# Optimization experiments

Hardware: AMD Instinct MI355X
Metric: run time of the kernel (lower is better)

Reference implementation:

```python
import jax, jax.numpy as jnp
import numpy as np

N_NODES = 100000
N_EDGES = 1200000
IN_CH = 64
HID = 16
OUT_CH = 64
EDGE_DIM = 3


def _glorot(key, shape):
    fan_in, fan_out = shape[0], shape[1]
    lim = float(np.sqrt(6.0 / (fan_in + fan_out)))
    return jax.random.uniform(key, shape, jnp.float32, -lim, lim)


def setup_inputs() -> dict:
    key = jax.random.key(0)
    ks = jax.random.split(key, 16)
    x = jax.random.normal(ks[0], (N_NODES, IN_CH), jnp.float32)
    edge_index = jax.random.randint(ks[1], (2, N_EDGES), 0, N_NODES, jnp.int64)
    edge_attr = jax.random.normal(ks[2], (N_EDGES, EDGE_DIM), jnp.float32)
    return {
        "x": x,
        "edge_index": edge_index,
        "edge_attr": edge_attr,
        # conv1: in->16
        "W1l": _glorot(ks[3], (IN_CH, HID)), "b1l": jnp.zeros((HID,), jnp.float32),
        "W1r": _glorot(ks[4], (IN_CH, HID)), "b1r": jnp.zeros((HID,), jnp.float32),
        "W1e": _glorot(ks[5], (EDGE_DIM, IN_CH)), "b1e": jnp.zeros((IN_CH,), jnp.float32),
        # conv2: 16->out
        "W2l": _glorot(ks[6], (HID, OUT_CH)), "b2l": jnp.zeros((OUT_CH,), jnp.float32),
        "W2r": _glorot(ks[7], (HID, OUT_CH)), "b2r": jnp.zeros((OUT_CH,), jnp.float32),
        "W2e": _glorot(ks[8], (EDGE_DIM, HID)), "b2e": jnp.zeros((HID,), jnp.float32),
    }


def _sage_conv(x, src, dst, edge_attr, We, be, Wl, bl, Wr, br):
    # message: neighbor feature + projected edge attribute (edge_dim-aware SAGE)
    msg = x[src] + edge_attr @ We + be                       # [E, C_in]
    agg = jax.ops.segment_sum(msg, dst, num_segments=N_NODES)  # [N, C_in]
    deg = jax.ops.segment_sum(jnp.ones((msg.shape[0],), msg.dtype), dst,
                              num_segments=N_NODES)
    agg = agg / jnp.maximum(deg, 1.0)[:, None]               # mean aggregation
    return agg @ Wl + bl + x @ Wr + br                       # neighbor + self paths


def reference(x, edge_index, edge_attr,
              W1l, b1l, W1r, b1r, W1e, b1e,
              W2l, b2l, W2r, b2r, W2e, b2e):
    src, dst = edge_index[0], edge_index[1]
    h = jax.nn.relu(_sage_conv(x, src, dst, edge_attr, W1e, b1e, W1l, b1l, W1r, b1r))
    # F.dropout(training=self.training): eval mode -> identity
    out = _sage_conv(h, src, dst, edge_attr, W2e, b2e, W2l, b2l, W2r, b2r)
    return out
```

## Files before the change

### kernel.cpp

```cpp
#include <hip/hip_runtime.h>
#include <hip/hip_bf16.h>
#include <stdint.h>

#define N_NODES 100000
#define N_EDGES 1200000
#define IN_CH 64
#define HID 16
#define OUT_CH 64

#define BN 100
#define NB 1000
#define BCAP 2048
#define CAP 2048
#define SC_EPB 4096
#define SC_TPB 512
#define SC_EPT (SC_EPB / SC_TPB)

typedef __hip_bfloat16 bf16;

__device__ __forceinline__ float b2f(bf16 v) { return __bfloat162float(v); }
__device__ __forceinline__ float lo_f(uint32_t p) { return __uint_as_float(p << 16); }
__device__ __forceinline__ float hi_f(uint32_t p) { return __uint_as_float(p & 0xffff0000u); }
__device__ __forceinline__ uint16_t f2bb(float v) {
    bf16 h = __float2bfloat16(v);
    return *reinterpret_cast<uint16_t*>(&h);
}

__device__ __forceinline__ float loadf(const void* p, size_t i, int bf) {
    return bf ? b2f(((const bf16*)p)[i]) : ((const float*)p)[i];
}
__device__ __forceinline__ uint32_t bfbits(const void* p, size_t i, int bf) {
    if (bf) return ((const uint16_t*)p)[i];
    return f2bb(((const float*)p)[i]);
}
__device__ __forceinline__ int ld_dst(const int* p, int j, int i64) {
    if (i64) return ((const int2*)p)[(size_t)N_EDGES + j].x;
    return p[(size_t)N_EDGES + j];
}
__device__ __forceinline__ int ld_src(const int* p, int j, int i64) {
    if (i64) return ((const int2*)p)[j].x;
    return p[j];
}

__device__ __forceinline__ int detect_bf(const void* x) {
    const uint16_t* u = (const uint16_t*)x;
    int cnt = 0;
    for (int i = 0; i < 64; ++i) {
        int e = (u[i] >> 7) & 0xff;
        cnt += (e >= 100 && e <= 140);
    }
    return cnt >= 50;
}
__device__ __forceinline__ int detect_i64(const int* ei) {
    const uint32_t* w = (const uint32_t*)ei;
    int z = 0;
    for (int i = 1; i < 64; i += 2) z += (w[i] == 0u);
    return z >= 16;
}

__global__ void __launch_bounds__(256) k_y(const void* __restrict__ x,
                                           const void* __restrict__ W1l,
                                           const void* __restrict__ W1r,
                                           const void* __restrict__ b1l,
                                           const void* __restrict__ b1r,
                                           const void* __restrict__ W1e,
                                           const void* __restrict__ b1e,
                                           bf16* __restrict__ y,
                                           bf16* __restrict__ zh,
                                           float* __restrict__ wc,
                                           int* __restrict__ gcnt) {
    __shared__ float w[IN_CH * 32];
    __shared__ float bz[HID];
    __shared__ int s_bf;
    if (threadIdx.x == 0) s_bf = detect_bf(x);
    __syncthreads();
    int bf = s_bf;
    for (int t = threadIdx.x; t < IN_CH * 32; t += 256) {
        int k = t >> 5, cc = t & 31;
        w[t] = (cc < 16) ? loadf(W1l, k * HID + cc, bf) : loadf(W1r, k * HID + (cc - 16), bf);
    }
    if (threadIdx.x < HID)
        bz[threadIdx.x] = loadf(b1l, threadIdx.x, bf) + loadf(b1r, threadIdx.x, bf);
    if (blockIdx.x == 0) {
        for (int i = threadIdx.x; i < NB; i += 256) gcnt[i] = 0;
    }
    __syncthreads();
    if (blockIdx.x == 0 && threadIdx.x < HID) {
        int j = threadIdx.x;
        float s0 = 0.f, s1 = 0.f, s2 = 0.f, s3 = 0.f;
        for (int k = 0; k < IN_CH; ++k) {
            float wl = w[k * 32 + j];
            s0 += loadf(W1e, k, bf) * wl;
            s1 += loadf(W1e, IN_CH + k, bf) * wl;
            s2 += loadf(W1e, 2 * IN_CH + k, bf) * wl;
            s3 += loadf(b1e, k, bf) * wl;
        }
        wc[j] = s0;
        wc[HID + j] = s1;
        wc[2 * HID + j] = s2;
        wc[3 * HID + j] = s3;
    }
    int tid = blockIdx.x * 256 + threadIdx.x;
    int row = tid >> 1;
    if (row >= N_NODES) return;
    int half = tid & 1, cs = half * 16;
    float acc[16];
#pragma unroll
    for (int j = 0; j < 16; ++j) acc[j] = 0.f;
    if (bf) {
        const uint4* xr = (const uint4*)((const uint16_t*)x + (size_t)row * IN_CH);
        uint4 q[8];
#pragma unroll
        for (int i = 0; i < 8; ++i) q[i] = xr[i];
        const uint32_t* qq = (const uint32_t*)q;
#pragma unroll
        for (int k2 = 0; k2 < 32; ++k2) {
            uint32_t u = qq[k2];
            float x0 = lo_f(u), x1 = hi_f(u);
            const float* w0 = &w[(2 * k2) * 32 + cs];
            const float* w1 = w0 + 32;
#pragma unroll
            for (int j = 0; j < 16; ++j) acc[j] += x0 * w0[j] + x1 * w1[j];
        }
    } else {
        const float4* xr = (const float4*)((const float*)x + (size_t)row * IN_CH);
#pragma unroll
        for (int c = 0; c < 4; ++c) {
            float4 f[4];
#pragma unroll
            for (int i = 0; i < 4; ++i) f[i] = xr[c * 4 + i];
            const float* ff = (const float*)f;
#pragma unroll
            for (int kk = 0; kk < 16; ++kk) {
                float xk = ff[kk];
                const float* wr = &w[(c * 16 + kk) * 32 + cs];
#pragma unroll
                for (int j = 0; j < 16; ++j) acc[j] += xk * wr[j];
            }
        }
    }
    if (half) {
#pragma unroll
        for (int j = 0; j < 16; ++j) acc[j] += bz[j];
    }
    uint32_t pk[8];
#pragma unroll
    for (int j2 = 0; j2 < 8; ++j2)
        pk[j2] = (uint32_t)f2bb(acc[2 * j2]) | ((uint32_t)f2bb(acc[2 * j2 + 1]) << 16);
    bf16* dst = half ? (zh + (size_t)row * HID) : (y + (size_t)row * HID);
    uint4* d4 = (uint4*)dst;
    d4[0] = make_uint4(pk[0], pk[1], pk[2], pk[3]);
    d4[1] = make_uint4(pk[4], pk[5], pk[6], pk[7]);
}

__global__ void __launch_bounds__(SC_TPB) k_bscatter(const void* __restrict__ x,
                                                     const int* __restrict__ ei,
                                                     const void* __restrict__ ea,
                                                     int* __restrict__ gcnt,
                                                     uint2* __restrict__ slots,
                                                     uint16_t* __restrict__ ea2v) {
    __shared__ int lhist[NB];
    __shared__ int lscan[NB];
    __shared__ int ldelta[NB];
    __shared__ int wsum[8];
    __shared__ int s_flags;
    __shared__ uint2 lval[SC_EPB];
    __shared__ uint16_t lea[SC_EPB];
    __shared__ uint16_t lbid[SC_EPB];
    int t = threadIdx.x;
    for (int i = t; i < NB; i += SC_TPB) lhist[i] = 0;
    if (t == 0) s_flags = detect_bf(x) | (detect_i64(ei) << 1);
    __syncthreads();
    int bf = s_flags & 1, i64 = (s_flags >> 1) & 1;
    int base = blockIdx.x * SC_EPB;
    uint32_t rb[SC_EPT], srcv[SC_EPT], ea01v[SC_EPT], ea2r[SC_EPT];
#pragma unroll
    for (int i = 0; i < SC_EPT; ++i) {
        int e = base + i * SC_TPB + t;
        rb[i] = 0xFFFFFFFFu;
        if (e < N_EDGES) {
            uint32_t d = (uint32_t)ld_dst(ei, e, i64);
            srcv[i] = (uint32_t)ld_src(ei, e, i64);
            ea01v[i] = bfbits(ea, (size_t)e * 3, bf) |
                       (bfbits(ea, (size_t)e * 3 + 1, bf) << 16);
            ea2r[i] = bfbits(ea, (size_t)e * 3 + 2, bf);
            uint32_t b = d / BN;
            uint32_t dl = d - b * BN;
            uint32_t r = (uint32_t)atomicAdd(&lhist[b], 1);
            rb[i] = (b << 19) | (dl << 12) | r;
        }
    }
    __syncthreads();
    int b0 = 2 * t, b1 = 2 * t + 1;
    int cnt0 = (b0 < NB) ? lhist[b0] : 0;
    int cnt1 = (b1 < NB) ? lhist[b1] : 0;
    int s_local = cnt0 + cnt1;
    int incl = s_local;
    int lane = t & 63;
#pragma unroll
    for (int d = 1; d < 64; d <<= 1) {
        int v = __shfl_up(incl, d);
        if (lane >= d) incl += v;
    }
    int w = t >> 6;
    if (lane == 63) wsum[w] = incl;
    __syncthreads();
    int wbase = 0, nst = 0;
#pragma unroll
    for (int i = 0; i < 8; ++i) {
        int v = wsum[i];
        wbase += (i < w) ? v : 0;
        nst += v;
    }
    int run = wbase + incl - s_local;
    if (b0 < NB) {
        lscan[b0] = run;
        if (cnt0) ldelta[b0] = b0 * BCAP + atomicAdd(&gcnt[b0], cnt0) - run;
    }
    run += cnt0;
    if (b1 < NB) {
        lscan[b1] = run;
        if (cnt1) ldelta[b1] = b1 * BCAP + atomicAdd(&gcnt[b1], cnt1) - run;
    }
    __syncthreads();
#pragma unroll
    for (int i = 0; i < SC_EPT; ++i) {
        if (rb[i] == 0xFFFFFFFFu) continue;
        uint32_t b = rb[i] >> 19;
        uint32_t dl = (rb[i] >> 12) & 0x7Fu;
        uint32_t r = rb[i] & 0xFFFu;
        int lp = lscan[b] + (int)r;
        lval[lp] = make_uint2(srcv[i] | (dl << 17), ea01v[i]);
        lea[lp] = (uint16_t)ea2r[i];
        lbid[lp] = (uint16_t)b;
    }
    __syncthreads();
    for (int p = t; p < nst; p += SC_TPB) {
        int b = lbid[p];
        int gp = ldelta[b] + p;
        slots[gp] = lval[p];
        ea2v[gp] = lea[p];
    }
}

#define SORT_CHUNK(nst)                                                        \
    {                                                                          \
        for (int i_ = t; i_ < (nst); i_ += 256)                                \
            atomicAdd(&hist[su[i_].x >> 17], 1);                               \
        __syncthreads();                                                       \
        if (t < 128) sbuf[t] = (t < BN) ? hist[t] : 0;                         \
        __syncthreads();                                                       \
        for (int off_ = 1; off_ < 128; off_ <<= 1) {                           \
            int v_ = 0;                                                        \
            if (t < 128 && t >= off_) v_ = sbuf[t - off_];                     \
            __syncthreads();                                                   \
            if (t < 128) sbuf[t] += v_;                                        \
            __syncthreads();                                                   \
        }                                                                      \
        if (t < BN) {                                                          \
            int ex_ = sbuf[t] - hist[t];                                       \
            noff[t] = ex_;                                                     \
            cur[t] = ex_;                                                      \
        }                                                                      \
        __syncthreads();                                                       \
        for (int i_ = t; i_ < (nst); i_ += 256) {                              \
            int r_ = atomicAdd(&cur[su[i_].x >> 17], 1);                       \
            sidx[r_] = (uint16_t)i_;                                           \
        }                                                                      \
        __syncthreads();                                                       \
    }

__global__ void __launch_bounds__(256) k_agg1(const uint2* __restrict__ slots,
                                              const uint16_t* __restrict__ ea2v,
                                              const int* __restrict__ gcnt,
                                              const bf16* __restrict__ y,
                                              const float* __restrict__ wc,
                                              bf16* __restrict__ zh,
                                              float* __restrict__ sa) {
    __shared__ uint2 su[CAP];
    __shared__ uint16_t ea2s[CAP];
    __shared__ uint16_t sidx[CAP];
    __shared__ int hist[BN], noff[BN], cur[BN], sbuf[128];
    __shared__ float swc[64];
    int t = threadIdx.x;
    if (t < 64) swc[t] = wc[t];
    int b = blockIdx.x;
    int n = gcnt[b];
    const uint2* sp = slots + (size_t)b * BCAP;
    const uint16_t* ep = ea2v + (size_t)b * BCAP;
    int dl = t >> 1, half = t & 1, cs = half * 8;
    float acc[8] = {0.f, 0.f, 0.f, 0.f, 0.f, 0.f, 0.f, 0.f};
    float a0 = 0.f, a1 = 0.f, a2 = 0.f, degT = 0.f;

    for (int base = 0; base < n; base += CAP) {
        int nst = n - base < CAP ? n - base : CAP;
        for (int i_ = t; i_ < BN; i_ += 256) hist[i_] = 0;
        for (int i_ = t; i_ < nst; i_ += 256) {
            su[i_] = sp[base + i_];
            ea2s[i_] = ep[base + i_];
        }
        __syncthreads();
        SORT_CHUNK(nst)
        if (dl < BN) {
            int kb = noff[dl];
            int ke = (dl == BN - 1) ? nst : noff[dl + 1];
            int k = kb;
            for (; k + 3 < ke; k += 4) {
                int i0 = sidx[k], i1 = sidx[k + 1], i2 = sidx[k + 2], i3 = sidx[k + 3];
                uint2 s0 = su[i0], s1 = su[i1], s2 = su[i2], s3 = su[i3];
                uint4 q0 = *(const uint4*)(y + (size_t)(s0.x & 0x1FFFFu) * HID + cs);
                uint4 q1 = *(const uint4*)(y + (size_t)(s1.x & 0x1FFFFu) * HID + cs);
                uint4 q2 = *(const uint4*)(y + (size_t)(s2.x & 0x1FFFFu) * HID + cs);
                uint4 q3 = *(const uint4*)(y + (size_t)(s3.x & 0x1FFFFu) * HID + cs);
                acc[0] += lo_f(q0.x) + lo_f(q1.x) + lo_f(q2.x) + lo_f(q3.x);
                acc[1] += hi_f(q0.x) + hi_f(q1.x) + hi_f(q2.x) + hi_f(q3.x);
                acc[2] += lo_f(q0.y) + lo_f(q1.y) + lo_f(q2.y) + lo_f(q3.y);
                acc[3] += hi_f(q0.y) + hi_f(q1.y) + hi_f(q2.y) + hi_f(q3.y);
                acc[4] += lo_f(q0.z) + lo_f(q1.z) + lo_f(q2.z) + lo_f(q3.z);
                acc[5] += hi_f(q0.z) + hi_f(q1.z) + hi_f(q2.z) + hi_f(q3.z);
                acc[6] += lo_f(q0.w) + lo_f(q1.w) + lo_f(q2.w) + lo_f(q3.w);
                acc[7] += hi_f(q0.w) + hi_f(q1.w) + hi_f(q2.w) + hi_f(q3.w);
                if (half == 0) {
                    a0 += lo_f(s0.y) + lo_f(s1.y) + lo_f(s2.y) + lo_f(s3.y);
                    a1 += hi_f(s0.y) + hi_f(s1.y) + hi_f(s2.y) + hi_f(s3.y);
                    a2 += __uint_as_float((uint32_t)ea2s[i0] << 16) +
                          __uint_as_float((uint32_t)ea2s[i1] << 16) +
                          __uint_as_float((uint32_t)ea2s[i2] << 16) +
                          __uint_as_float((uint32_t)ea2s[i3] << 16);
                }
            }
            for (; k < ke; ++k) {
                int i0 = sidx[k];
                uint2 s0 = su[i0];
                uint4 q0 = *(const uint4*)(y + (size_t)(s0.x & 0x1FFFFu) * HID + cs);
                acc[0] += lo_f(q0.x); acc[1] += hi_f(q0.x);
                acc[2] += lo_f(q0.y); acc[3] += hi_f(q0.y);
                acc[4] += lo_f(q0.z); acc[5] += hi_f(q0.z);
                acc[6] += lo_f(q0.w); acc[7] += hi_f(q0.w);
                if (half == 0) {
                    a0 += lo_f(s0.y);
                    a1 += hi_f(s0.y);
                    a2 += __uint_as_float((uint32_t)ea2s[i0] << 16);
                }
            }
            degT += (float)hist[dl];
        }
        __syncthreads();
    }
    if (dl < BN) {
        a0 += __shfl_xor(a0, 1);
        a1 += __shfl_xor(a1, 1);
        a2 += __shfl_xor(a2, 1);
        size_t i = (size_t)b * BN + dl;
        float inv = 1.0f / fmaxf(degT, 1.0f);
        uint4 zq = *(const uint4*)(zh + i * HID + cs);
        float zf[8] = {lo_f(zq.x), hi_f(zq.x), lo_f(zq.y), hi_f(zq.y),
                       lo_f(zq.z), hi_f(zq.z), lo_f(zq.w), hi_f(zq.w)};
        uint32_t pk[4];
#pragma unroll
        for (int j = 0; j < 4; ++j) {
            float t0 = (acc[2 * j] + a0 * swc[cs + 2 * j] + a1 * swc[16 + cs + 2 * j] +
                        a2 * swc[32 + cs + 2 * j] + degT * swc[48 + cs + 2 * j]) * inv;
            float t1 = (acc[2 * j + 1] + a0 * swc[cs + 2 * j + 1] + a1 * swc[17 + cs + 2 * j] +
                        a2 * swc[33 + cs + 2 * j] + degT * swc[49 + cs + 2 * j]) * inv;
            float h0 = fmaxf(t0 + zf[2 * j], 0.f);
            float h1 = fmaxf(t1 + zf[2 * j + 1], 0.f);
            pk[j] = (uint32_t)f2bb(h0) | ((uint32_t)f2bb(h1) << 16);
        }
        *(uint4*)(zh + i * HID + cs) = make_uint4(pk[0], pk[1], pk[2], pk[3]);
        if (half == 0) {
            sa[i * 3 + 0] = a0;
            sa[i * 3 + 1] = a1;
            sa[i * 3 + 2] = a2;
        }
    }
}

__global__ void __launch_bounds__(256) k_agg2(const void* __restrict__ x,
                                              const uint2* __restrict__ slots,
                                              const int* __restrict__ gcnt,
                                              const bf16* __restrict__ zh,
                                              const float* __restrict__ sa,
                                              const void* __restrict__ W2l,
                                              const void* __restrict__ b2l,
                                              const void* __restrict__ W2r,
                                              const void* __restrict__ b2r,
                                              const void* __restrict__ W2e,
                                              const void* __restrict__ b2e,
                                              void* __restrict__ out) {
    __shared__ uint2 su[CAP];
    __shared__ uint16_t sidx[CAP];
    __shared__ int hist[BN], noff[BN], cur[BN], sbuf[128];
    __shared__ float facc[BN * HID];
    __shared__ bf16 hl[BN * HID];
    __shared__ float w2l[HID * OUT_CH];
    __shared__ float w2r[HID * OUT_CH];
    __shared__ float swe[3 * HID];
    __shared__ float sbe[HID];
    __shared__ float sbb[OUT_CH];
    __shared__ int s_bf;
    int t = threadIdx.x;
    if (t == 0) s_bf = detect_bf(x);
    __syncthreads();
    int bf = s_bf;
    for (int i = t; i < HID * OUT_CH; i += 256) {
        w2l[i] = loadf(W2l, i, bf);
        w2r[i] = loadf(W2r, i, bf);
    }
    if (t < 3 * HID) swe[t] = loadf(W2e, t, bf);
    if (t < HID) sbe[t] = loadf(b2e, t, bf);
    if (t < OUT_CH) sbb[t] = loadf(b2l, t, bf) + loadf(b2r, t, bf);
    int b = blockIdx.x;
    int n = gcnt[b];
    const uint2* sp = slots + (size_t)b * BCAP;
    int dl = t >> 1, half = t & 1, cs = half * 8;
    float acc[8] = {0.f, 0.f, 0.f, 0.f, 0.f, 0.f, 0.f, 0.f};
    float degT = 0.f;

    for (int base = 0; base < n; base += CAP) {
        int nst = n - base < CAP ? n - base : CAP;
        for (int i_ = t; i_ < BN; i_ += 256) hist[i_] = 0;
        for (int i_ = t; i_ < nst; i_ += 256) su[i_] = sp[base + i_];
        __syncthreads();
        SORT_CHUNK(nst)
        if (dl < BN) {
            int kb = noff[dl];
            int ke = (dl == BN - 1) ? nst : noff[dl + 1];
            int k = kb;
            for (; k + 3 < ke; k += 4) {
                int i0 = sidx[k], i1 = sidx[k + 1], i2 = sidx[k + 2], i3 = sidx[k + 3];
                uint2 s0 = su[i0], s1 = su[i1], s2 = su[i2], s3 = su[i3];
                uint4 q0 = *(const uint4*)(zh + (size_t)(s0.x & 0x1FFFFu) * HID + cs);
                uint4 q1 = *(const uint4*)(zh + (size_t)(s1.x & 0x1FFFFu) * HID + cs);
                uint4 q2 = *(const uint4*)(zh + (size_t)(s2.x & 0x1FFFFu) * HID + cs);
                uint4 q3 = *(const uint4*)(zh + (size_t)(s3.x & 0x1FFFFu) * HID + cs);
                acc[0] += lo_f(q0.x) + lo_f(q1.x) + lo_f(q2.x) + lo_f(q3.x);
                acc[1] += hi_f(q0.x) + hi_f(q1.x) + hi_f(q2.x) + hi_f(q3.x);
                acc[2] += lo_f(q0.y) + lo_f(q1.y) + lo_f(q2.y) + lo_f(q3.y);
                acc[3] += hi_f(q0.y) + hi_f(q1.y) + hi_f(q2.y) + hi_f(q3.y);
                acc[4] += lo_f(q0.z) + lo_f(q1.z) + lo_f(q2.z) + lo_f(q3.z);
                acc[5] += hi_f(q0.z) + hi_f(q1.z) + hi_f(q2.z) + hi_f(q3.z);
                acc[6] += lo_f(q0.w) + lo_f(q1.w) + lo_f(q2.w) + lo_f(q3.w);
                acc[7] += hi_f(q0.w) + hi_f(q1.w) + hi_f(q2.w) + hi_f(q3.w);
            }
            for (; k < ke; ++k) {
                uint2 s0 = su[sidx[k]];
                uint4 q0 = *(const uint4*)(zh + (size_t)(s0.x & 0x1FFFFu) * HID + cs);
                acc[0] += lo_f(q0.x); acc[1] += hi_f(q0.x);
                acc[2] += lo_f(q0.y); acc[3] += hi_f(q0.y);
                acc[4] += lo_f(q0.z); acc[5] += hi_f(q0.z);
                acc[6] += lo_f(q0.w); acc[7] += hi_f(q0.w);
            }
            degT += (float)hist[dl];
        }
        __syncthreads();
    }
    if (dl < BN) {
        size_t i = (size_t)b * BN + dl;
        float inv = 1.0f / fmaxf(degT, 1.0f);
        float a0 = sa[i * 3 + 0], a1 = sa[i * 3 + 1], a2 = sa[i * 3 + 2];
        float4 f0, f1;
        float* fo = (float*)&f0;
        float* f1o = (float*)&f1;
#pragma unroll
        for (int j = 0; j < 4; ++j) {
            fo[j] = (acc[j] + a0 * swe[cs + j] + a1 * swe[16 + cs + j] +
                     a2 * swe[32 + cs + j] + degT * sbe[cs + j]) * inv;
            f1o[j] = (acc[4 + j] + a0 * swe[cs + 4 + j] + a1 * swe[16 + cs + 4 + j] +
                      a2 * swe[32 + cs + 4 + j] + degT * sbe[cs + 4 + j]) * inv;
        }
        *(float4*)&facc[dl * HID + cs] = f0;
        *(float4*)&facc[dl * HID + cs + 4] = f1;
        *(uint4*)&hl[dl * HID + cs] = *(const uint4*)(zh + i * HID + cs);
    }
    __syncthreads();
    for (int idx = t; idx < BN * OUT_CH; idx += 256) {
        int dli = idx >> 6, j = idx & 63;
        size_t i = (size_t)b * BN + dli;
        float o = sbb[j];
#pragma unroll
        for (int cc = 0; cc < HID; ++cc)
            o += facc[dli * HID + cc] * w2l[cc * OUT_CH + j] +
                 b2f(hl[dli * HID + cc]) * w2r[cc * OUT_CH + j];
        if (bf)
            ((bf16*)out)[i * OUT_CH + j] = __float2bfloat16(o);
        else
            ((float*)out)[i * OUT_CH + j] = o;
    }
}

extern "C" void kernel_launch(void* const* d_in, const int* in_sizes, int n_in,
                              void* d_out, int out_size, void* d_ws, size_t ws_size,
                              hipStream_t stream) {
    const void* x   = d_in[0];
    const int*  ei  = (const int*)d_in[1];
    const void* ea  = d_in[2];
    const void* W1l = d_in[3];
    const void* b1l = d_in[4];
    const void* W1r = d_in[5];
    const void* b1r = d_in[6];
    const void* W1e = d_in[7];
    const void* b1e = d_in[8];
    const void* W2l = d_in[9];
    const void* b2l = d_in[10];
    const void* W2r = d_in[11];
    const void* b2r = d_in[12];
    const void* W2e = d_in[13];
    const void* b2e = d_in[14];

    const size_t N16 = (size_t)N_NODES * HID;
    char* p = (char*)d_ws;
    uint2*    slots  = (uint2*)p;    p += (size_t)NB * BCAP * sizeof(uint2);
    uint16_t* ea2v   = (uint16_t*)p; p += (size_t)NB * BCAP * sizeof(uint16_t);
    bf16*     y      = (bf16*)p;     p += N16 * sizeof(bf16);
    bf16*     zh     = (bf16*)p;     p += N16 * sizeof(bf16);
    float*    sa     = (float*)p;    p += (size_t)3 * N_NODES * sizeof(float);
    int*      gcnt   = (int*)p;      p += NB * sizeof(int);
    float*    wc     = (float*)p;    p += 64 * sizeof(float);

    k_y<<<((size_t)N_NODES * 2 + 255) / 256, 256, 0, stream>>>(x, W1l, W1r, b1l, b1r,
                                                               W1e, b1e, y, zh, wc, gcnt);
    k_bscatter<<<(N_EDGES + SC_EPB - 1) / SC_EPB, SC_TPB, 0, stream>>>(x, ei, ea, gcnt,
                                                                       slots, ea2v);
    k_agg1<<<NB, 256, 0, stream>>>(slots, ea2v, gcnt, y, wc, zh, sa);
    k_agg2<<<NB, 256, 0, stream>>>(x, slots, gcnt, zh, sa, W2l, b2l, W2r, b2r,
                                   W2e, b2e, d_out);
}
```

Baseline: 200.8 us.

## Fuse node projection with edge bucketing and reuse sorted sources in layer two

Merges the node-projection kernel and the edge bucket-scatter kernel into one launch, with blocks interleaved by role (2 projection, 3 scatter per group) and a shared memory pool. The gcnt zeroing becomes a memset. The first aggregation kernel now writes its per-bucket sorted source list and node offsets to global memory, so the second aggregation skips reloading slots and re-sorting. The per-bucket chunk loop is dropped in favour of clamping counts to CAP. This trades an extra global write/read of the sorted arrays for removing one launch and the second sort, and silently truncates buckets with more than CAP edges.

New measurement: 194.0 us. 1.04x faster.

```diff
diff --git a/kernel.cpp b/kernel.cpp
--- a/kernel.cpp
+++ b/kernel.cpp
@@ -12,9 +12,13 @@
 #define NB 1000
 #define BCAP 2048
 #define CAP 2048
-#define SC_EPB 4096
-#define SC_TPB 512
-#define SC_EPT (SC_EPB / SC_TPB)
+
+#define F_TPB 512
+#define KY_BLOCKS ((N_NODES * 2 + F_TPB - 1) / F_TPB)
+#define SC_EPB 2048
+#define SC_EPT (SC_EPB / F_TPB)
+#define SC_BLOCKS ((N_EDGES + SC_EPB - 1) / SC_EPB)
+#define F_GROUPS 196
 
 typedef __hip_bfloat16 bf16;
 
@@ -58,125 +62,127 @@
     return z >= 16;
 }
 
-__global__ void __launch_bounds__(256) k_y(const void* __restrict__ x,
-                                           const void* __restrict__ W1l,
-                                           const void* __restrict__ W1r,
-                                           const void* __restrict__ b1l,
-                                           const void* __restrict__ b1r,
-                                           const void* __restrict__ W1e,
-                                           const void* __restrict__ b1e,
-                                           bf16* __restrict__ y,
-                                           bf16* __restrict__ zh,
-                                           float* __restrict__ wc,
-                                           int* __restrict__ gcnt) {
-    __shared__ float w[IN_CH * 32];
-    __shared__ float bz[HID];
-    __shared__ int s_bf;
-    if (threadIdx.x == 0) s_bf = detect_bf(x);
-    __syncthreads();
-    int bf = s_bf;
-    for (int t = threadIdx.x; t < IN_CH * 32; t += 256) {
-        int k = t >> 5, cc = t & 31;
-        w[t] = (cc < 16) ? loadf(W1l, k * HID + cc, bf) : loadf(W1r, k * HID + (cc - 16), bf);
-    }
-    if (threadIdx.x < HID)
-        bz[threadIdx.x] = loadf(b1l, threadIdx.x, bf) + loadf(b1r, threadIdx.x, bf);
-    if (blockIdx.x == 0) {
-        for (int i = threadIdx.x; i < NB; i += 256) gcnt[i] = 0;
-    }
-    __syncthreads();
-    if (blockIdx.x == 0 && threadIdx.x < HID) {
-        int j = threadIdx.x;
-        float s0 = 0.f, s1 = 0.f, s2 = 0.f, s3 = 0.f;
-        for (int k = 0; k < IN_CH; ++k) {
-            float wl = w[k * 32 + j];
-            s0 += loadf(W1e, k, bf) * wl;
-            s1 += loadf(W1e, IN_CH + k, bf) * wl;
-            s2 += loadf(W1e, 2 * IN_CH + k, bf) * wl;
-            s3 += loadf(b1e, k, bf) * wl;
-        }
-        wc[j] = s0;
-        wc[HID + j] = s1;
-        wc[2 * HID + j] = s2;
-        wc[3 * HID + j] = s3;
-    }
-    int tid = blockIdx.x * 256 + threadIdx.x;
-    int row = tid >> 1;
-    if (row >= N_NODES) return;
-    int half = tid & 1, cs = half * 16;
-    float acc[16];
-#pragma unroll
-    for (int j = 0; j < 16; ++j) acc[j] = 0.f;
-    if (bf) {
-        const uint4* xr = (const uint4*)((const uint16_t*)x + (size_t)row * IN_CH);
-        uint4 q[8];
-#pragma unroll
-        for (int i = 0; i < 8; ++i) q[i] = xr[i];
-        const uint32_t* qq = (const uint32_t*)q;
-#pragma unroll
-        for (int k2 = 0; k2 < 32; ++k2) {
-            uint32_t u = qq[k2];
-            float x0 = lo_f(u), x1 = hi_f(u);
-            const float* w0 = &w[(2 * k2) * 32 + cs];
-            const float* w1 = w0 + 32;
-#pragma unroll
-            for (int j = 0; j < 16; ++j) acc[j] += x0 * w0[j] + x1 * w1[j];
-        }
-    } else {
-        const float4* xr = (const float4*)((const float*)x + (size_t)row * IN_CH);
-#pragma unroll
-        for (int c = 0; c < 4; ++c) {
-            float4 f[4];
-#pragma unroll
-            for (int i = 0; i < 4; ++i) f[i] = xr[c * 4 + i];
-            const float* ff = (const float*)f;
-#pragma unroll
-            for (int kk = 0; kk < 16; ++kk) {
-                float xk = ff[kk];
-                const float* wr = &w[(c * 16 + kk) * 32 + cs];
-#pragma unroll
-                for (int j = 0; j < 16; ++j) acc[j] += xk * wr[j];
-            }
-        }
-    }
-    if (half) {
-#pragma unroll
-        for (int j = 0; j < 16; ++j) acc[j] += bz[j];
-    }
-    uint32_t pk[8];
-#pragma unroll
-    for (int j2 = 0; j2 < 8; ++j2)
-        pk[j2] = (uint32_t)f2bb(acc[2 * j2]) | ((uint32_t)f2bb(acc[2 * j2 + 1]) << 16);
-    bf16* dst = half ? (zh + (size_t)row * HID) : (y + (size_t)row * HID);
-    uint4* d4 = (uint4*)dst;
-    d4[0] = make_uint4(pk[0], pk[1], pk[2], pk[3]);
-    d4[1] = make_uint4(pk[4], pk[5], pk[6], pk[7]);
-}
-
-__global__ void __launch_bounds__(SC_TPB) k_bscatter(const void* __restrict__ x,
-                                                     const int* __restrict__ ei,
-                                                     const void* __restrict__ ea,
-                                                     int* __restrict__ gcnt,
-                                                     uint2* __restrict__ slots,
-                                                     uint16_t* __restrict__ ea2v) {
-    __shared__ int lhist[NB];
-    __shared__ int lscan[NB];
-    __shared__ int ldelta[NB];
+__global__ void __launch_bounds__(F_TPB) k_fused(const void* __restrict__ x,
+                                                 const int* __restrict__ ei,
+                                                 const void* __restrict__ ea,
+                                                 const void* __restrict__ W1l,
+                                                 const void* __restrict__ W1r,
+                                                 const void* __restrict__ b1l,
+                                                 const void* __restrict__ b1r,
+                                                 const void* __restrict__ W1e,
+                                                 const void* __restrict__ b1e,
+                                                 bf16* __restrict__ y,
+                                                 bf16* __restrict__ zh,
+                                                 float* __restrict__ wc,
+                                                 int* __restrict__ gcnt,
+                                                 uint2* __restrict__ slots,
+                                                 uint16_t* __restrict__ ea2v) {
+    __shared__ __align__(16) char smem[36608];
     __shared__ int wsum[8];
     __shared__ int s_flags;
-    __shared__ uint2 lval[SC_EPB];
-    __shared__ uint16_t lea[SC_EPB];
-    __shared__ uint16_t lbid[SC_EPB];
     int t = threadIdx.x;
-    for (int i = t; i < NB; i += SC_TPB) lhist[i] = 0;
+    int g = blockIdx.x / 5, r = blockIdx.x % 5;
     if (t == 0) s_flags = detect_bf(x) | (detect_i64(ei) << 1);
+
+    if (r < 2) {
+        int kyid = g * 2 + r;
+        if (kyid >= KY_BLOCKS) return;
+        float* w = (float*)smem;
+        float* bz = (float*)(smem + 8192);
+        __syncthreads();
+        int bf = s_flags & 1;
+        for (int i = t; i < IN_CH * 32; i += F_TPB) {
+            int k = i >> 5, cc = i & 31;
+            w[i] = (cc < 16) ? loadf(W1l, k * HID + cc, bf)
+                             : loadf(W1r, k * HID + (cc - 16), bf);
+        }
+        if (t < HID) bz[t] = loadf(b1l, t, bf) + loadf(b1r, t, bf);
+        __syncthreads();
+        if (kyid == 0 && t < HID) {
+            int j = t;
+            float s0 = 0.f, s1 = 0.f, s2 = 0.f, s3 = 0.f;
+            for (int k = 0; k < IN_CH; ++k) {
+                float wl = w[k * 32 + j];
+                s0 += loadf(W1e, k, bf) * wl;
+                s1 += loadf(W1e, IN_CH + k, bf) * wl;
+                s2 += loadf(W1e, 2 * IN_CH + k, bf) * wl;
+                s3 += loadf(b1e, k, bf) * wl;
+            }
+            wc[j] = s0;
+            wc[HID + j] = s1;
+            wc[2 * HID + j] = s2;
+            wc[3 * HID + j] = s3;
+        }
+        int tid = kyid * F_TPB + t;
+        int row = tid >> 1;
+        if (row >= N_NODES) return;
+        int half = tid & 1, cs = half * 16;
+        float acc[16];
+#pragma unroll
+        for (int j = 0; j < 16; ++j) acc[j] = 0.f;
+        if (bf) {
+            const uint4* xr = (const uint4*)((const uint16_t*)x + (size_t)row * IN_CH);
+            uint4 q[8];
+#pragma unroll
+            for (int i = 0; i < 8; ++i) q[i] = xr[i];
+            const uint32_t* qq = (const uint32_t*)q;
+#pragma unroll
+            for (int k2 = 0; k2 < 32; ++k2) {
+                uint32_t u = qq[k2];
+                float x0 = lo_f(u), x1 = hi_f(u);
+                const float* w0 = &w[(2 * k2) * 32 + cs];
+                const float* w1 = w0 + 32;
+#pragma unroll
+                for (int j = 0; j < 16; ++j) acc[j] += x0 * w0[j] + x1 * w1[j];
+            }
+        } else {
+            const float4* xr = (const float4*)((const float*)x + (size_t)row * IN_CH);
+#pragma unroll
+            for (int c = 0; c < 4; ++c) {
+                float4 f[4];
+#pragma unroll
+                for (int i = 0; i < 4; ++i) f[i] = xr[c * 4 + i];
+                const float* ff = (const float*)f;
+#pragma unroll
+                for (int kk = 0; kk < 16; ++kk) {
+                    float xk = ff[kk];
+                    const float* wr = &w[(c * 16 + kk) * 32 + cs];
+#pragma unroll
+                    for (int j = 0; j < 16; ++j) acc[j] += xk * wr[j];
+                }
+            }
+        }
+        if (half) {
+#pragma unroll
+            for (int j = 0; j < 16; ++j) acc[j] += bz[j];
+        }
+        uint32_t pk[8];
+#pragma unroll
+        for (int j2 = 0; j2 < 8; ++j2)
+            pk[j2] = (uint32_t)f2bb(acc[2 * j2]) | ((uint32_t)f2bb(acc[2 * j2 + 1]) << 16);
+        bf16* dst = half ? (zh + (size_t)row * HID) : (y + (size_t)row * HID);
+        uint4* d4 = (uint4*)dst;
+        d4[0] = make_uint4(pk[0], pk[1], pk[2], pk[3]);
+        d4[1] = make_uint4(pk[4], pk[5], pk[6], pk[7]);
+        return;
+    }
+
+    int scid = g * 3 + (r - 2);
+    if (scid >= SC_BLOCKS) return;
+    uint2* lval = (uint2*)smem;
+    int* lhist = (int*)(smem + 16384);
+    int* lscan = (int*)(smem + 20384);
+    int* ldelta = (int*)(smem + 24384);
+    uint16_t* lea = (uint16_t*)(smem + 28384);
+    uint16_t* lbid = (uint16_t*)(smem + 32480);
+    for (int i = t; i < NB; i += F_TPB) lhist[i] = 0;
     __syncthreads();
     int bf = s_flags & 1, i64 = (s_flags >> 1) & 1;
-    int base = blockIdx.x * SC_EPB;
+    int base = scid * SC_EPB;
     uint32_t rb[SC_EPT], srcv[SC_EPT], ea01v[SC_EPT], ea2r[SC_EPT];
 #pragma unroll
     for (int i = 0; i < SC_EPT; ++i) {
-        int e = base + i * SC_TPB + t;
+        int e = base + i * F_TPB + t;
         rb[i] = 0xFFFFFFFFu;
         if (e < N_EDGES) {
             uint32_t d = (uint32_t)ld_dst(ei, e, i64);
@@ -186,8 +192,8 @@
             ea2r[i] = bfbits(ea, (size_t)e * 3 + 2, bf);
             uint32_t b = d / BN;
             uint32_t dl = d - b * BN;
-            uint32_t r = (uint32_t)atomicAdd(&lhist[b], 1);
-            rb[i] = (b << 19) | (dl << 12) | r;
+            uint32_t rr = (uint32_t)atomicAdd(&lhist[b], 1);
+            rb[i] = (b << 19) | (dl << 12) | rr;
         }
     }
     __syncthreads();
@@ -228,14 +234,14 @@
         if (rb[i] == 0xFFFFFFFFu) continue;
         uint32_t b = rb[i] >> 19;
         uint32_t dl = (rb[i] >> 12) & 0x7Fu;
-        uint32_t r = rb[i] & 0xFFFu;
-        int lp = lscan[b] + (int)r;
+        uint32_t rr = rb[i] & 0xFFFu;
+        int lp = lscan[b] + (int)rr;
         lval[lp] = make_uint2(srcv[i] | (dl << 17), ea01v[i]);
         lea[lp] = (uint16_t)ea2r[i];
         lbid[lp] = (uint16_t)b;
     }
     __syncthreads();
-    for (int p = t; p < nst; p += SC_TPB) {
+    for (int p = t; p < nst; p += F_TPB) {
         int b = lbid[p];
         int gp = ldelta[b] + p;
         slots[gp] = lval[p];
@@ -276,7 +282,9 @@
                                               const bf16* __restrict__ y,
                                               const float* __restrict__ wc,
                                               bf16* __restrict__ zh,
-                                              float* __restrict__ sa) {
+                                              float* __restrict__ sa,
+                                              uint32_t* __restrict__ ssrc,
+                                              int* __restrict__ nof2) {
     __shared__ uint2 su[CAP];
     __shared__ uint16_t ea2s[CAP];
     __shared__ uint16_t sidx[CAP];
@@ -286,66 +294,65 @@
     if (t < 64) swc[t] = wc[t];
     int b = blockIdx.x;
     int n = gcnt[b];
+    if (n > CAP) n = CAP;
     const uint2* sp = slots + (size_t)b * BCAP;
     const uint16_t* ep = ea2v + (size_t)b * BCAP;
     int dl = t >> 1, half = t & 1, cs = half * 8;
     float acc[8] = {0.f, 0.f, 0.f, 0.f, 0.f, 0.f, 0.f, 0.f};
     float a0 = 0.f, a1 = 0.f, a2 = 0.f, degT = 0.f;
 
-    for (int base = 0; base < n; base += CAP) {
-        int nst = n - base < CAP ? n - base : CAP;
-        for (int i_ = t; i_ < BN; i_ += 256) hist[i_] = 0;
-        for (int i_ = t; i_ < nst; i_ += 256) {
-            su[i_] = sp[base + i_];
-            ea2s[i_] = ep[base + i_];
-        }
-        __syncthreads();
-        SORT_CHUNK(nst)
-        if (dl < BN) {
-            int kb = noff[dl];
-            int ke = (dl == BN - 1) ? nst : noff[dl + 1];
-            int k = kb;
-            for (; k + 3 < ke; k += 4) {
-                int i0 = sidx[k], i1 = sidx[k + 1], i2 = sidx[k + 2], i3 = sidx[k + 3];
-                uint2 s0 = su[i0], s1 = su[i1], s2 = su[i2], s3 = su[i3];
-                uint4 q0 = *(const uint4*)(y + (size_t)(s0.x & 0x1FFFFu) * HID + cs);
-                uint4 q1 = *(const uint4*)(y + (size_t)(s1.x & 0x1FFFFu) * HID + cs);
-                uint4 q2 = *(const uint4*)(y + (size_t)(s2.x & 0x1FFFFu) * HID + cs);
-                uint4 q3 = *(const uint4*)(y + (size_t)(s3.x & 0x1FFFFu) * HID + cs);
-                acc[0] += lo_f(q0.x) + lo_f(q1.x) + lo_f(q2.x) + lo_f(q3.x);
-                acc[1] += hi_f(q0.x) + hi_f(q1.x) + hi_f(q2.x) + hi_f(q3.x);
-                acc[2] += lo_f(q0.y) + lo_f(q1.y) + lo_f(q2.y) + lo_f(q3.y);
-                acc[3] += hi_f(q0.y) + hi_f(q1.y) + hi_f(q2.y) + hi_f(q3.y);
-                acc[4] += lo_f(q0.z) + lo_f(q1.z) + lo_f(q2.z) + lo_f(q3.z);
-                acc[5] += hi_f(q0.z) + hi_f(q1.z) + hi_f(q2.z) + hi_f(q3.z);
-                acc[6] += lo_f(q0.w) + lo_f(q1.w) + lo_f(q2.w) + lo_f(q3.w);
-                acc[7] += hi_f(q0.w) + hi_f(q1.w) + hi_f(q2.w) + hi_f(q3.w);
-                if (half == 0) {
-                    a0 += lo_f(s0.y) + lo_f(s1.y) + lo_f(s2.y) + lo_f(s3.y);
-                    a1 += hi_f(s0.y) + hi_f(s1.y) + hi_f(s2.y) + hi_f(s3.y);
-                    a2 += __uint_as_float((uint32_t)ea2s[i0] << 16) +
-                          __uint_as_float((uint32_t)ea2s[i1] << 16) +
-                          __uint_as_float((uint32_t)ea2s[i2] << 16) +
-                          __uint_as_float((uint32_t)ea2s[i3] << 16);
-                }
+    for (int i_ = t; i_ < BN; i_ += 256) hist[i_] = 0;
+    for (int i_ = t; i_ < n; i_ += 256) {
+        su[i_] = sp[i_];
+        ea2s[i_] = ep[i_];
+    }
+    __syncthreads();
+    SORT_CHUNK(n)
+    for (int p = t; p < n; p += 256) ssrc[(size_t)b * BCAP + p] = su[sidx[p]].x;
+    if (t < BN) nof2[b * 128 + t] = noff[t];
+    if (dl < BN) {
+        int kb = noff[dl];
+        int ke = (dl == BN - 1) ? n : noff[dl + 1];
+        int k = kb;
+        for (; k + 3 < ke; k += 4) {
+            int i0 = sidx[k], i1 = sidx[k + 1], i2 = sidx[k + 2], i3 = sidx[k + 3];
+            uint2 s0 = su[i0], s1 = su[i1], s2 = su[i2], s3 = su[i3];
+            uint4 q0 = *(const uint4*)(y + (size_t)(s0.x & 0x1FFFFu) * HID + cs);
+            uint4 q1 = *(const uint4*)(y + (size_t)(s1.x & 0x1FFFFu) * HID + cs);
+            uint4 q2 = *(const uint4*)(y + (size_t)(s2.x & 0x1FFFFu) * HID + cs);
+            uint4 q3 = *(const uint4*)(y + (size_t)(s3.x & 0x1FFFFu) * HID + cs);
+            acc[0] += lo_f(q0.x) + lo_f(q1.x) + lo_f(q2.x) + lo_f(q3.x);
+            acc[1] += hi_f(q0.x) + hi_f(q1.x) + hi_f(q2.x) + hi_f(q3.x);
+            acc[2] += lo_f(q0.y) + lo_f(q1.y) + lo_f(q2.y) + lo_f(q3.y);
+            acc[3] += hi_f(q0.y) + hi_f(q1.y) + hi_f(q2.y) + hi_f(q3.y);
+            acc[4] += lo_f(q0.z) + lo_f(q1.z) + lo_f(q2.z) + lo_f(q3.z);
+            acc[5] += hi_f(q0.z) + hi_f(q1.z) + hi_f(q2.z) + hi_f(q3.z);
+            acc[6] += lo_f(q0.w) + lo_f(q1.w) + lo_f(q2.w) + lo_f(q3.w);
+            acc[7] += hi_f(q0.w) + hi_f(q1.w) + hi_f(q2.w) + hi_f(q3.w);
+            if (half == 0) {
+                a0 += lo_f(s0.y) + lo_f(s1.y) + lo_f(s2.y) + lo_f(s3.y);
+                a1 += hi_f(s0.y) + hi_f(s1.y) + hi_f(s2.y) + hi_f(s3.y);
+                a2 += __uint_as_float((uint32_t)ea2s[i0] << 16) +
+                      __uint_as_float((uint32_t)ea2s[i1] << 16) +
+                      __uint_as_float((uint32_t)ea2s[i2] << 16) +
+                      __uint_as_float((uint32_t)ea2s[i3] << 16);
             }
-            for (; k < ke; ++k) {
-                int i0 = sidx[k];
-                uint2 s0 = su[i0];
-                uint4 q0 = *(const uint4*)(y + (size_t)(s0.x & 0x1FFFFu) * HID + cs);
-                acc[0] += lo_f(q0.x); acc[1] += hi_f(q0.x);
-                acc[2] += lo_f(q0.y); acc[3] += hi_f(q0.y);
-                acc[4] += lo_f(q0.z); acc[5] += hi_f(q0.z);
-                acc[6] += lo_f(q0.w); acc[7] += hi_f(q0.w);
-                if (half == 0) {
-                    a0 += lo_f(s0.y);
-                    a1 += hi_f(s0.y);
-                    a2 += __uint_as_float((uint32_t)ea2s[i0] << 16);
-                }
+        }
+        for (; k < ke; ++k) {
+            int i0 = sidx[k];
+            uint2 s0 = su[i0];
+            uint4 q0 = *(const uint4*)(y + (size_t)(s0.x & 0x1FFFFu) * HID + cs);
+            acc[0] += lo_f(q0.x); acc[1] += hi_f(q0.x);
+            acc[2] += lo_f(q0.y); acc[3] += hi_f(q0.y);
+            acc[4] += lo_f(q0.z); acc[5] += hi_f(q0.z);
+            acc[6] += lo_f(q0.w); acc[7] += hi_f(q0.w);
+            if (half == 0) {
+                a0 += lo_f(s0.y);
+                a1 += hi_f(s0.y);
+                a2 += __uint_as_float((uint32_t)ea2s[i0] << 16);
             }
-            degT += (float)hist[dl];
-        }
-        __syncthreads();
+        }
+        degT = (float)hist[dl];
     }
     if (dl < BN) {
         a0 += __shfl_xor(a0, 1);
@@ -377,7 +384,8 @@
 }
 
 __global__ void __launch_bounds__(256) k_agg2(const void* __restrict__ x,
-                                              const uint2* __restrict__ slots,
+                                              const uint32_t* __restrict__ ssrc,
+                                              const int* __restrict__ nof2,
                                               const int* __restrict__ gcnt,
                                               const bf16* __restrict__ zh,
                                               const float* __restrict__ sa,
@@ -388,9 +396,8 @@
                                               const void* __restrict__ W2e,
                                               const void* __restrict__ b2e,
                                               void* __restrict__ out) {
-    __shared__ uint2 su[CAP];
-    __shared__ uint16_t sidx[CAP];
-    __shared__ int hist[BN], noff[BN], cur[BN], sbuf[128];
+    __shared__ uint32_t ss[CAP];
+    __shared__ int snoff[BN];
     __shared__ float facc[BN * HID];
     __shared__ bf16 hl[BN * HID];
     __shared__ float w2l[HID * OUT_CH];
@@ -412,48 +419,41 @@
     if (t < OUT_CH) sbb[t] = loadf(b2l, t, bf) + loadf(b2r, t, bf);
     int b = blockIdx.x;
     int n = gcnt[b];
-    const uint2* sp = slots + (size_t)b * BCAP;
+    if (n > CAP) n = CAP;
+    for (int i = t; i < n; i += 256) ss[i] = ssrc[(size_t)b * BCAP + i];
+    if (t < BN) snoff[t] = nof2[b * 128 + t];
+    __syncthreads();
     int dl = t >> 1, half = t & 1, cs = half * 8;
     float acc[8] = {0.f, 0.f, 0.f, 0.f, 0.f, 0.f, 0.f, 0.f};
     float degT = 0.f;
-
-    for (int base = 0; base < n; base += CAP) {
-        int nst = n - base < CAP ? n - base : CAP;
-        for (int i_ = t; i_ < BN; i_ += 256) hist[i_] = 0;
-        for (int i_ = t; i_ < nst; i_ += 256) su[i_] = sp[base + i_];
-        __syncthreads();
-        SORT_CHUNK(nst)
-        if (dl < BN) {
-            int kb = noff[dl];
-            int ke = (dl == BN - 1) ? nst : noff[dl + 1];
-            int k = kb;
-            for (; k + 3 < ke; k += 4) {
-                int i0 = sidx[k], i1 = sidx[k + 1], i2 = sidx[k + 2], i3 = sidx[k + 3];
-                uint2 s0 = su[i0], s1 = su[i1], s2 = su[i2], s3 = su[i3];
-                uint4 q0 = *(const uint4*)(zh + (size_t)(s0.x & 0x1FFFFu) * HID + cs);
-                uint4 q1 = *(const uint4*)(zh + (size_t)(s1.x & 0x1FFFFu) * HID + cs);
-                uint4 q2 = *(const uint4*)(zh + (size_t)(s2.x & 0x1FFFFu) * HID + cs);
-                uint4 q3 = *(const uint4*)(zh + (size_t)(s3.x & 0x1FFFFu) * HID + cs);
-                acc[0] += lo_f(q0.x) + lo_f(q1.x) + lo_f(q2.x) + lo_f(q3.x);
-                acc[1] += hi_f(q0.x) + hi_f(q1.x) + hi_f(q2.x) + hi_f(q3.x);
-                acc[2] += lo_f(q0.y) + lo_f(q1.y) + lo_f(q2.y) + lo_f(q3.y);
-                acc[3] += hi_f(q0.y) + hi_f(q1.y) + hi_f(q2.y) + hi_f(q3.y);
-                acc[4] += lo_f(q0.z) + lo_f(q1.z) + lo_f(q2.z) + lo_f(q3.z);
-                acc[5] += hi_f(q0.z) + hi_f(q1.z) + hi_f(q2.z) + hi_f(q3.z);
-                acc[6] += lo_f(q0.w) + lo_f(q1.w) + lo_f(q2.w) + lo_f(q3.w);
-                acc[7] += hi_f(q0.w) + hi_f(q1.w) + hi_f(q2.w) + hi_f(q3.w);
-            }
-            for (; k < ke; ++k) {
-                uint2 s0 = su[sidx[k]];
-                uint4 q0 = *(const uint4*)(zh + (size_t)(s0.x & 0x1FFFFu) * HID + cs);
-                acc[0] += lo_f(q0.x); acc[1] += hi_f(q0.x);
-                acc[2] += lo_f(q0.y); acc[3] += hi_f(q0.y);
-                acc[4] += lo_f(q0.z); acc[5] += hi_f(q0.z);
-                acc[6] += lo_f(q0.w); acc[7] += hi_f(q0.w);
-            }
-            degT += (float)hist[dl];
-        }
-        __syncthreads();
+    if (dl < BN) {
+        int kb = snoff[dl];
+        int ke = (dl == BN - 1) ? n : snoff[dl + 1];
+        degT = (float)(ke - kb);
+        int k = kb;
+        for (; k + 3 < ke; k += 4) {
+            uint32_t s0 = ss[k], s1 = ss[k + 1], s2 = ss[k + 2], s3 = ss[k + 3];
+            uint4 q0 = *(const uint4*)(zh + (size_t)(s0 & 0x1FFFFu) * HID + cs);
+            uint4 q1 = *(const uint4*)(zh + (size_t)(s1 & 0x1FFFFu) * HID + cs);
+            uint4 q2 = *(const uint4*)(zh + (size_t)(s2 & 0x1FFFFu) * HID + cs);
+            uint4 q3 = *(const uint4*)(zh + (size_t)(s3 & 0x1FFFFu) * HID + cs);
+            acc[0] += lo_f(q0.x) + lo_f(q1.x) + lo_f(q2.x) + lo_f(q3.x);
+            acc[1] += hi_f(q0.x) + hi_f(q1.x) + hi_f(q2.x) + hi_f(q3.x);
+            acc[2] += lo_f(q0.y) + lo_f(q1.y) + lo_f(q2.y) + lo_f(q3.y);
+            acc[3] += hi_f(q0.y) + hi_f(q1.y) + hi_f(q2.y) + hi_f(q3.y);
+            acc[4] += lo_f(q0.z) + lo_f(q1.z) + lo_f(q2.z) + lo_f(q3.z);
+            acc[5] += hi_f(q0.z) + hi_f(q1.z) + hi_f(q2.z) + hi_f(q3.z);
+            acc[6] += lo_f(q0.w) + lo_f(q1.w) + lo_f(q2.w) + lo_f(q3.w);
+            acc[7] += hi_f(q0.w) + hi_f(q1.w) + hi_f(q2.w) + hi_f(q3.w);
+        }
+        for (; k < ke; ++k) {
+            uint32_t s0 = ss[k];
+            uint4 q0 = *(const uint4*)(zh + (size_t)(s0 & 0x1FFFFu) * HID + cs);
+            acc[0] += lo_f(q0.x); acc[1] += hi_f(q0.x);
+            acc[2] += lo_f(q0.y); acc[3] += hi_f(q0.y);
+            acc[4] += lo_f(q0.z); acc[5] += hi_f(q0.z);
+            acc[6] += lo_f(q0.w); acc[7] += hi_f(q0.w);
+        }
     }
     if (dl < BN) {
         size_t i = (size_t)b * BN + dl;
@@ -510,19 +510,20 @@
 
     const size_t N16 = (size_t)N_NODES * HID;
     char* p = (char*)d_ws;
-    uint2*    slots  = (uint2*)p;    p += (size_t)NB * BCAP * sizeof(uint2);
-    uint16_t* ea2v   = (uint16_t*)p; p += (size_t)NB * BCAP * sizeof(uint16_t);
-    bf16*     y      = (bf16*)p;     p += N16 * sizeof(bf16);
-    bf16*     zh     = (bf16*)p;     p += N16 * sizeof(bf16);
-    float*    sa     = (float*)p;    p += (size_t)3 * N_NODES * sizeof(float);
-    int*      gcnt   = (int*)p;      p += NB * sizeof(int);
-    float*    wc     = (float*)p;    p += 64 * sizeof(float);
-
-    k_y<<<((size_t)N_NODES * 2 + 255) / 256, 256, 0, stream>>>(x, W1l, W1r, b1l, b1r,
-                                                               W1e, b1e, y, zh, wc, gcnt);
-    k_bscatter<<<(N_EDGES + SC_EPB - 1) / SC_EPB, SC_TPB, 0, stream>>>(x, ei, ea, gcnt,
-                                                                       slots, ea2v);
-    k_agg1<<<NB, 256, 0, stream>>>(slots, ea2v, gcnt, y, wc, zh, sa);
-    k_agg2<<<NB, 256, 0, stream>>>(x, slots, gcnt, zh, sa, W2l, b2l, W2r, b2r,
+    uint2*    slots = (uint2*)p;    p += (size_t)NB * BCAP * sizeof(uint2);
+    uint16_t* ea2v  = (uint16_t*)p; p += (size_t)NB * BCAP * sizeof(uint16_t);
+    uint32_t* ssrc  = (uint32_t*)p; p += (size_t)NB * BCAP * sizeof(uint32_t);
+    int*      nof2  = (int*)p;      p += (size_t)NB * 128 * sizeof(int);
+    bf16*     y     = (bf16*)p;     p += N16 * sizeof(bf16);
+    bf16*     zh    = (bf16*)p;     p += N16 * sizeof(bf16);
+    float*    sa    = (float*)p;    p += (size_t)3 * N_NODES * sizeof(float);
+    int*      gcnt  = (int*)p;      p += NB * sizeof(int);
+    float*    wc    = (float*)p;    p += 64 * sizeof(float);
+
+    hipMemsetAsync(gcnt, 0, NB * sizeof(int), stream);
+    k_fused<<<F_GROUPS * 5, F_TPB, 0, stream>>>(x, ei, ea, W1l, W1r, b1l, b1r, W1e, b1e,
+                                                y, zh, wc, gcnt, slots, ea2v);
+    k_agg1<<<NB, 256, 0, stream>>>(slots, ea2v, gcnt, y, wc, zh, sa, ssrc, nof2);
+    k_agg2<<<NB, 256, 0, stream>>>(x, ssrc, nof2, gcnt, zh, sa, W2l, b2l, W2r, b2r,
                                    W2e, b2e, d_out);
 }
```
